# Performance work log

Hardware: AMD Instinct MI355X
Metric: run time of the kernel (lower is better)

Reference implementation:

```python
import jax, jax.numpy as jnp
import numpy as np

T, B, N, C, H, D = 4, 8, 1024, 512, 8, 64
EPS = 1e-5


def setup_inputs() -> dict:
    key = jax.random.key(0)
    ks = jax.random.split(key, 16)
    d = {"x": jax.random.normal(ks[0], (T, B, N, C), jnp.float32)}
    for i, nm in enumerate(["q", "k", "v", "p"]):
        kW, kmu, kvar = jax.random.split(ks[1 + i], 3)
        d[f"W{nm}"] = jax.random.normal(kW, (C, C), jnp.float32) * 0.02
        d[f"b{nm}"] = jnp.zeros((C,), jnp.float32)
        d[f"g{nm}"] = jnp.ones((C,), jnp.float32)
        d[f"beta{nm}"] = jnp.zeros((C,), jnp.float32)
        d[f"mu{nm}"] = jax.random.normal(kmu, (C,), jnp.float32) * 0.1
        d[f"var{nm}"] = jax.random.uniform(kvar, (C,), jnp.float32, 0.5, 1.5)
    return d


def _lin_bn(z, W, b, g, beta, mu, var):
    # nn.Linear over channel dim, then eval-mode BatchNorm1d per channel
    y = jnp.einsum('tbnc,dc->tbnd', z, W) + b
    return (y - mu) * (g * jax.lax.rsqrt(var + EPS)) + beta


def _to_heads(z):
    # (t,b,n,c) -> (t,b,h,n,d)
    return z.reshape(T, B, N, H, D).transpose(0, 1, 3, 2, 4)


def reference(x, Wq, bq, gq, betaq, muq, varq,
              Wk, bk, gk, betak, muk, vark,
              Wv, bv, gv, betav, muv, varv,
              Wp, bp, gp, betap, mup, varp):
    q = _to_heads(_lin_bn(x, Wq, bq, gq, betaq, muq, varq))
    k = _to_heads(_lin_bn(x, Wk, bk, gk, betak, muk, vark))
    v = _to_heads(_lin_bn(x, Wv, bv, gv, betav, muv, varv))
    # attention_linear variant: kv = (k^T @ v) / N ; y = q @ kv
    kv = jnp.einsum('tbhnd,tbhne->tbhde', k, v) / float(N)  # (t,b,h,d,d)
    y = jnp.einsum('tbhnd,tbhde->tbhne', q, kv)             # (t,b,h,n,d)
    y = y.transpose(0, 1, 3, 2, 4).reshape(T, B, N, C)
    return _lin_bn(y, Wp, bp, gp, betap, mup, varp)
```

## Files before the change

### kernel.cpp

```cpp
#include <hip/hip_runtime.h>

#define T_ 4
#define B_ 8
#define N_ 1024
#define C_ 512
#define H_ 8
#define D_ 64
#define M_ (T_*B_*N_)
#define TB_ (T_*B_)

typedef __bf16 bf16;
typedef __bf16 bf16x4 __attribute__((ext_vector_type(4)));
typedef __bf16 bf16x8 __attribute__((ext_vector_type(8)));
typedef float f32x4 __attribute__((ext_vector_type(4)));

__device__ __forceinline__ void gload16(const void* g, void* l) {
  __builtin_amdgcn_global_load_lds(
      (const __attribute__((address_space(1))) void*)g,
      (__attribute__((address_space(3))) void*)l, 16, 0, 0);
}

struct PtrPack { const float* p[24]; };

__global__ __launch_bounds__(256)
void prep_all(PtrPack pk, bf16* __restrict__ WB, float* __restrict__ BS) {
  const int mat = blockIdx.x >> 9, d = blockIdx.x & 511;
  const float* W    = pk.p[6*mat + 0];
  const float* b    = pk.p[6*mat + 1];
  const float* g    = pk.p[6*mat + 2];
  const float* beta = pk.p[6*mat + 3];
  const float* mu   = pk.p[6*mat + 4];
  const float* var  = pk.p[6*mat + 5];
  float s = g[d] * rsqrtf(var[d] + 1e-5f);
  if (threadIdx.x == 0) BS[mat*512 + d] = (b[d] - mu[d]) * s + beta[d];
  bf16* Wout = WB + (size_t)mat * 262144 + (size_t)d * 512;
  for (int c = threadIdx.x; c < 512; c += 256)
    Wout[c] = (bf16)(W[(size_t)d * 512 + c] * s);
}

__global__ __launch_bounds__(256)
void prep_wqT(const float* __restrict__ W, const float* __restrict__ g,
              const float* __restrict__ var, bf16* __restrict__ WqT) {
  const int di = blockIdx.x >> 3, ci = blockIdx.x & 7;
  const int t = threadIdx.x;
  __shared__ float lds[64][65];
  const int rgrp = t >> 4, k = t & 15;
#pragma unroll
  for (int p = 0; p < 4; p++) {
    int r = p * 16 + rgrp;
    int d = di * 64 + r;
    float s = g[d] * rsqrtf(var[d] + 1e-5f);
    float4 v = *(const float4*)(W + (size_t)d * 512 + ci * 64 + k * 4);
    lds[r][k*4+0] = v.x * s; lds[r][k*4+1] = v.y * s;
    lds[r][k*4+2] = v.z * s; lds[r][k*4+3] = v.w * s;
  }
  __syncthreads();
#pragma unroll
  for (int p = 0; p < 16; p++) {
    int c = p * 4 + (t >> 6), dd = t & 63;
    WqT[(size_t)(ci*64 + c) * 512 + di*64 + dd] = (bf16)lds[dd][c];
  }
}

__global__ __launch_bounds__(256)
void cvt_x_t(const float* __restrict__ x, bf16* __restrict__ xb,
             bf16* __restrict__ xT, float* __restrict__ spart) {
  const int bid = blockIdx.x;
  const int tb = bid >> 7, nc = (bid >> 3) & 15, cc = bid & 7;
  const int t = threadIdx.x;
  __shared__ float lds[64][65];
  __shared__ float sred[16][64];
  const float* xbase = x + (size_t)tb * 524288 + (size_t)nc * 64 * 512 + cc * 64;
  bf16* xbb = xb + (size_t)tb * 524288 + (size_t)nc * 64 * 512 + cc * 64;
  bf16* xTb = xT + (size_t)tb * 524288 + (size_t)(cc * 64) * 1024 + nc * 64;
  const int rgrp = t >> 4, k = t & 15;
  float s0 = 0, s1 = 0, s2 = 0, s3 = 0;
#pragma unroll
  for (int p = 0; p < 4; p++) {
    int r = p * 16 + rgrp;
    float4 v = *(const float4*)(xbase + (size_t)r * 512 + k * 4);
    bf16x4 o; o[0]=(bf16)v.x; o[1]=(bf16)v.y; o[2]=(bf16)v.z; o[3]=(bf16)v.w;
    *(bf16x4*)(xbb + (size_t)r * 512 + k * 4) = o;
    lds[r][k*4+0]=v.x; lds[r][k*4+1]=v.y; lds[r][k*4+2]=v.z; lds[r][k*4+3]=v.w;
    s0 += v.x; s1 += v.y; s2 += v.z; s3 += v.w;
  }
  sred[rgrp][k*4+0]=s0; sred[rgrp][k*4+1]=s1; sred[rgrp][k*4+2]=s2; sred[rgrp][k*4+3]=s3;
  __syncthreads();
#pragma unroll
  for (int p = 0; p < 16; p++) {
    int c = p * 4 + (t >> 6), n = t & 63;
    xTb[(size_t)c * 1024 + n] = (bf16)lds[n][c];
  }
  if (t < 64) {
    float tot = 0;
#pragma unroll
    for (int rg = 0; rg < 16; rg++) tot += sred[rg][t];
    spart[(size_t)((tb*8 + cc)*16 + nc) * 64 + t] = tot;
  }
}

__global__ __launch_bounds__(512)
void ksvs(const bf16* __restrict__ WB, const float* __restrict__ spart,
          float* __restrict__ ksv) {
  const int tb = blockIdx.x, m = blockIdx.y;
  const int c = threadIdx.x, cc = c >> 6, cl = c & 63;
  __shared__ float sl[512];
  float tot = 0;
#pragma unroll
  for (int ncf = 0; ncf < 16; ncf++)
    tot += spart[(size_t)((tb*8 + cc)*16 + ncf) * 64 + cl];
  sl[c] = tot;
  __syncthreads();
  const bf16* Wrow = WB + (size_t)(m + 1) * 262144 + (size_t)c * 512;
  float acc = 0;
  for (int k = 0; k < 512; k += 8) {
    bf16x8 wv = *(const bf16x8*)(Wrow + k);
#pragma unroll
    for (int i = 0; i < 8; i++) acc += (float)wv[i] * sl[k + i];
  }
  ksv[m * 16384 + tb * 512 + c] = acc;
}

template <int NKT, int MT, int NT, bool BF16OUT, bool BIAS2, bool SYM>
__global__ __launch_bounds__(256)
void gemm2(const bf16* __restrict__ Abase, size_t Astr,
           const bf16* __restrict__ Btbase, size_t Btstr,
           const float* __restrict__ BSb, const float* __restrict__ cpart,
           bf16* __restrict__ ob, float* __restrict__ of, size_t Ostr) {
  constexpr int K = NKT * 64;
  constexpr int PERB = SYM ? (MT * (MT + 1) / 2) : (MT * NT);
  const int bid = blockIdx.x;
  const int xcd = bid & 7, j9 = bid >> 3;
  const int bat = xcd + 8 * (j9 / PERB);
  const int tile = j9 % PERB;
  int mi, ni;
  if constexpr (SYM) {
    if (tile < 4)      { mi = 0; ni = tile; }
    else if (tile < 7) { mi = 1; ni = tile - 3; }
    else if (tile < 9) { mi = 2; ni = tile - 5; }
    else               { mi = 3; ni = 3; }
  } else { mi = tile / NT; ni = tile % NT; }
  const bf16* A = Abase + (size_t)bat * Astr;
  const bf16* Bt = Btbase + (size_t)bat * Btstr;
  const int m0 = mi * 128, n0 = ni * 128;
  __shared__ __align__(16) bf16 As[2][128][64];
  __shared__ __align__(16) bf16 Bs[2][128][64];
  const int tid = threadIdx.x, w = tid >> 6, l = tid & 63;
  const int wm = w >> 1, wn = w & 1;
  const int lr = l & 15, lq = l >> 4, l7 = l & 7, lh = l >> 3;
  const int srcc = (l7 ^ lh) * 8;
  f32x4 acc[4][4] = {};

#define STG2(buf, kt)                                                         \
  { _Pragma("unroll") for (int i_ = 0; i_ < 4; i_++) {                        \
      int rb_ = w * 32 + i_ * 8;                                              \
      gload16(A  + (size_t)(m0 + rb_ + lh) * K + (kt) * 64 + srcc,            \
              &As[buf][rb_][0]);                                              \
      gload16(Bt + (size_t)(n0 + rb_ + lh) * K + (kt) * 64 + srcc,            \
              &Bs[buf][rb_][0]); } }

  STG2(0, 0);
  __syncthreads();
  for (int kt = 0; kt < NKT; kt++) {
    const int cur = kt & 1;
    if (kt + 1 < NKT) STG2(cur ^ 1, kt + 1);
    bf16x8 af[4][2], bv[4][2];
#pragma unroll
    for (int f = 0; f < 4; f++) {
      int ra = wm * 64 + f * 16 + lr, rb2 = wn * 64 + f * 16 + lr;
#pragma unroll
      for (int s = 0; s < 2; s++) {
        af[f][s] = *(const bf16x8*)&As[cur][ra][((s*4+lq) ^ (ra & 7)) * 8];
        bv[f][s] = *(const bf16x8*)&Bs[cur][rb2][((s*4+lq) ^ (rb2 & 7)) * 8];
      }
    }
#pragma unroll
    for (int mt = 0; mt < 4; mt++)
#pragma unroll
      for (int nt = 0; nt < 4; nt++)
#pragma unroll
        for (int s = 0; s < 2; s++)
          acc[mt][nt] = __builtin_amdgcn_mfma_f32_16x16x32_bf16(
              af[mt][s], bv[nt][s], acc[mt][nt], 0, 0, 0);
    __syncthreads();
  }
#undef STG2

  const int ldo = NT * 128;
#pragma unroll
  for (int mt = 0; mt < 4; mt++)
#pragma unroll
    for (int nt = 0; nt < 4; nt++) {
      int j = n0 + wn * 64 + nt * 16 + lr;
      float bj = 0.f;
      if constexpr (BIAS2) {
        bj = BSb[1536 + j];
#pragma unroll
        for (int h = 0; h < 8; h++)
          bj += cpart[(size_t)(bat * 8 + h) * 512 + j];
      }
      size_t mrow = (size_t)m0 + wm * 64 + mt * 16 + lq * 4;
#pragma unroll
      for (int r = 0; r < 4; r++) {
        if constexpr (BF16OUT)
          ob[(size_t)bat * Ostr + (mrow + r) * ldo + j] = (bf16)(acc[mt][nt][r] + bj);
        else
          of[(size_t)bat * Ostr + (mrow + r) * ldo + j] = acc[mt][nt][r] + bj;
      }
    }

  if constexpr (SYM) {
    if (mi != ni) {
      bf16* TB = (bf16*)As;
      __syncthreads();
#pragma unroll
      for (int mt = 0; mt < 4; mt++)
#pragma unroll
        for (int nt = 0; nt < 4; nt++) {
          int a = wn * 64 + nt * 16 + lr;
#pragma unroll
          for (int r = 0; r < 4; r++) {
            int b = wm * 64 + mt * 16 + lq * 4 + r;
            TB[(a * 128 + b) ^ ((a & 7) << 3)] = (bf16)acc[mt][nt][r];
          }
        }
      __syncthreads();
      const int a = tid >> 1, half = tid & 1;
#pragma unroll
      for (int i = 0; i < 4; i++) {
        int a2 = a + (i >> 1) * 64;
        int c8 = half * 8 + (i & 1) * 4;
        (void)a2; (void)c8;
      }
#pragma unroll
      for (int i = 0; i < 8; i++) {
        int rowa = tid >> 1;
        int c8 = half * 8 + i;
        bf16x8 v = *(const bf16x8*)&TB[(rowa * 128 + c8 * 8) ^ ((rowa & 7) << 3)];
        *(bf16x8*)(ob + (size_t)bat * Ostr + (size_t)(ni * 128 + rowa) * ldo +
                   mi * 128 + c8 * 8) = v;
      }
    }
  }
}

__global__ __launch_bounds__(256)
void kvz(const bf16* __restrict__ KGb, const bf16* __restrict__ WB,
         const float* __restrict__ BS, const float* __restrict__ ksv,
         bf16* __restrict__ ZT, float* __restrict__ cpart) {
  const int gid = blockIdx.x, tb = gid >> 3, h = gid & 7;
  const int t = threadIdx.x, w = t >> 6, l = t & 63;
  const int lr = l & 15, lq = l >> 4;
  __shared__ __align__(16) char lds[65536 + 65536 + 8192];
  bf16* bufA = (bf16*)lds;
  bf16* bufV = (bf16*)(lds + 65536);
  bf16* kvb  = (bf16*)(lds + 131072);

#pragma unroll
  for (int i = 0; i < 16; i++) {
    int r = i * 4 + w;
    gload16(KGb + (size_t)tb * 262144 + (size_t)(64*h + r) * 512 + ((l ^ (r & 7)) * 8),
            bufA + r * 512);
    gload16(WB + 2u * 262144 + (size_t)(64*h + r) * 512 + ((l ^ (r & 7)) * 8),
            bufV + r * 512);
  }
  __syncthreads();

  f32x4 acc2[4][4] = {};
#pragma unroll
  for (int ks = 0; ks < 4; ks++) {
    int gch = w * 16 + ks * 4 + lq;
    bf16x8 af2[4], bv2[4];
#pragma unroll
    for (int mf = 0; mf < 4; mf++) {
      int d = mf * 16 + lr;
      af2[mf] = *(const bf16x8*)&bufA[d * 512 + ((gch ^ (d & 7)) * 8)];
    }
#pragma unroll
    for (int nf = 0; nf < 4; nf++) {
      int e = nf * 16 + lr;
      bv2[nf] = *(const bf16x8*)&bufV[e * 512 + ((gch ^ (e & 7)) * 8)];
    }
#pragma unroll
    for (int mf = 0; mf < 4; mf++)
#pragma unroll
      for (int nf = 0; nf < 4; nf++)
        acc2[mf][nf] = __builtin_amdgcn_mfma_f32_16x16x32_bf16(
            af2[mf], bv2[nf], acc2[mf][nf], 0, 0, 0);
  }
  __syncthreads();

  float* part = (float*)lds + w * 4096;
#pragma unroll
  for (int mf = 0; mf < 4; mf++)
#pragma unroll
    for (int nf = 0; nf < 4; nf++)
#pragma unroll
      for (int r = 0; r < 4; r++) {
        int d = mf * 16 + lq * 4 + r, e = nf * 16 + lr;
        part[d * 64 + e] = acc2[mf][nf][r];
      }
  __syncthreads();
  {
    const float inv = 1.f / 1024.f;
    const float* pb = (const float*)lds;
#pragma unroll
    for (int jj = 0; jj < 16; jj++) {
      int flat = jj * 256 + t, d = flat >> 6, e = flat & 63;
      float s = pb[flat] + pb[4096 + flat] + pb[8192 + flat] + pb[12288 + flat];
      float ksh = ksv[tb * 512 + 64*h + d];
      float vsh = ksv[16384 + tb * 512 + 64*h + e];
      float bkh = BS[512 + 64*h + d];
      float bvh = BS[1024 + 64*h + e];
      float kv = (s + ksh * bvh + bkh * vsh) * inv + bkh * bvh;
      kvb[d * 64 + (((e >> 3) ^ (d & 7)) * 8 + (e & 7))] = (bf16)kv;
    }
  }
  __syncthreads();

#pragma unroll
  for (int i = 0; i < 16; i++) {
    int rb = i * 32 + w * 8;
    int r = rb + (l >> 3);
    gload16(WB + 3u * 262144 + (size_t)r * 512 + 64*h + (((l & 7) ^ (r & 7)) * 8),
            bufA + rb * 64);
  }
  __syncthreads();

  f32x4 acc3[4][8] = {};
#pragma unroll
  for (int s = 0; s < 2; s++) {
    bf16x8 af3[4];
#pragma unroll
    for (int mf = 0; mf < 4; mf++) {
      int d = mf * 16 + lr;
      af3[mf] = *(const bf16x8*)&kvb[d * 64 + (((s*4+lq) ^ (d & 7)) * 8)];
    }
#pragma unroll
    for (int nf = 0; nf < 8; nf++) {
      int jj = w * 128 + nf * 16 + lr;
      bf16x8 b3 = *(const bf16x8*)&bufA[jj * 64 + (((s*4+lq) ^ (jj & 7)) * 8)];
#pragma unroll
      for (int mf = 0; mf < 4; mf++)
        acc3[mf][nf] = __builtin_amdgcn_mfma_f32_16x16x32_bf16(
            af3[mf], b3, acc3[mf][nf], 0, 0, 0);
    }
  }

  bf16* zbase = ZT + (size_t)tb * 262144 + 64*h;
#pragma unroll
  for (int nf = 0; nf < 8; nf++) {
    int jj = w * 128 + nf * 16 + lr;
    float cp = 0.f;
#pragma unroll
    for (int mf = 0; mf < 4; mf++) {
      bf16x4 o;
#pragma unroll
      for (int r = 0; r < 4; r++) {
        o[r] = (bf16)acc3[mf][nf][r];
        cp += acc3[mf][nf][r] * BS[64*h + mf*16 + lq*4 + r];
      }
      *(bf16x4*)(zbase + (size_t)jj * 512 + mf * 16 + lq * 4) = o;
    }
    cp += __shfl_xor(cp, 16);
    cp += __shfl_xor(cp, 32);
    if (lq == 0) cpart[(size_t)(tb * 8 + h) * 512 + jj] = cp;
  }
}

extern "C" void kernel_launch(void* const* d_in, const int* in_sizes, int n_in,
                              void* d_out, int out_size, void* d_ws, size_t ws_size,
                              hipStream_t stream) {
  const float* x = (const float*)d_in[0];
  char* ws = (char*)d_ws;
  bf16*  xb    = (bf16*)(ws + 0);
  bf16*  xT    = (bf16*)(ws + 33554432);
  bf16*  Gb    = (bf16*)(ws + 67108864);
  bf16*  KGb   = (bf16*)(ws + 83886080);
  bf16*  ZT    = (bf16*)(ws + 100663296);
  bf16*  VT    = (bf16*)(ws + 117440512);
  bf16*  WB    = (bf16*)(ws + 134217728);
  bf16*  WqT   = (bf16*)(ws + 136314880);
  float* BS    = (float*)(ws + 136839168);
  float* ksv   = (float*)(ws + 136847360);
  float* cpart = (float*)(ws + 136978432);
  float* spart = (float*)(ws + 137502720);
  (void)in_sizes; (void)n_in; (void)out_size; (void)ws_size;

  PtrPack pk;
  for (int i = 0; i < 24; i++) pk.p[i] = (const float*)d_in[1 + i];

  prep_all<<<2048, 256, 0, stream>>>(pk, WB, BS);
  prep_wqT<<<64, 256, 0, stream>>>((const float*)d_in[1], (const float*)d_in[3],
                                   (const float*)d_in[6], WqT);
  cvt_x_t<<<4096, 256, 0, stream>>>(x, xb, xT, spart);
  ksvs<<<dim3(32, 2), 512, 0, stream>>>(WB, spart, ksv);
  gemm2<16, 4, 4, true, false, true><<<320, 256, 0, stream>>>(
      xT, 524288, xT, 524288, nullptr, nullptr, Gb, nullptr, 262144);
  gemm2<8, 4, 4, true, false, false><<<512, 256, 0, stream>>>(
      WB + 262144, 0, Gb, 262144, nullptr, nullptr, KGb, nullptr, 262144);
  kvz<<<256, 256, 0, stream>>>(KGb, WB, BS, ksv, ZT, cpart);
  gemm2<8, 4, 4, true, false, false><<<512, 256, 0, stream>>>(
      ZT, 262144, WqT, 0, nullptr, nullptr, VT, nullptr, 262144);
  gemm2<8, 8, 4, false, true, false><<<1024, 256, 0, stream>>>(
      xb, 524288, VT, 262144, BS, cpart, nullptr, (float*)d_out, 524288);
}
```

Before: 149.7 us.

## Drop LDS double buffering in GEMMs and use 512-thread 256x128 final GEMM

The batched GEMM kernel switches from double-buffered LDS staging to a single buffer with load, sync, compute, sync per k-step. This halves LDS use per block so more blocks can be resident. The final output GEMM moves to a new 512-thread kernel with 256x128 tiles, which reuses each B tile across twice as many rows and hoists the bias sums out of the store loop. The cost is that load latency is no longer overlapped with MFMA work inside a block, so hiding it now relies on occupancy.

```diff
diff --git a/kernel.cpp b/kernel.cpp
--- a/kernel.cpp
+++ b/kernel.cpp
@@ -121,12 +121,11 @@
   ksv[m * 16384 + tb * 512 + c] = acc;
 }
 
-template <int NKT, int MT, int NT, bool BF16OUT, bool BIAS2, bool SYM>
+template <int NKT, int MT, int NT, bool BF16OUT, bool SYM>
 __global__ __launch_bounds__(256)
-void gemm2(const bf16* __restrict__ Abase, size_t Astr,
-           const bf16* __restrict__ Btbase, size_t Btstr,
-           const float* __restrict__ BSb, const float* __restrict__ cpart,
-           bf16* __restrict__ ob, float* __restrict__ of, size_t Ostr) {
+void gemm_b(const bf16* __restrict__ Abase, size_t Astr,
+            const bf16* __restrict__ Btbase, size_t Btstr,
+            bf16* __restrict__ ob, float* __restrict__ of, size_t Ostr) {
   constexpr int K = NKT * 64;
   constexpr int PERB = SYM ? (MT * (MT + 1) / 2) : (MT * NT);
   const int bid = blockIdx.x;
@@ -143,35 +142,29 @@
   const bf16* A = Abase + (size_t)bat * Astr;
   const bf16* Bt = Btbase + (size_t)bat * Btstr;
   const int m0 = mi * 128, n0 = ni * 128;
-  __shared__ __align__(16) bf16 As[2][128][64];
-  __shared__ __align__(16) bf16 Bs[2][128][64];
+  __shared__ __align__(16) bf16 As[128][64];
+  __shared__ __align__(16) bf16 Bs[128][64];
   const int tid = threadIdx.x, w = tid >> 6, l = tid & 63;
   const int wm = w >> 1, wn = w & 1;
   const int lr = l & 15, lq = l >> 4, l7 = l & 7, lh = l >> 3;
   const int srcc = (l7 ^ lh) * 8;
   f32x4 acc[4][4] = {};
-
-#define STG2(buf, kt)                                                         \
-  { _Pragma("unroll") for (int i_ = 0; i_ < 4; i_++) {                        \
-      int rb_ = w * 32 + i_ * 8;                                              \
-      gload16(A  + (size_t)(m0 + rb_ + lh) * K + (kt) * 64 + srcc,            \
-              &As[buf][rb_][0]);                                              \
-      gload16(Bt + (size_t)(n0 + rb_ + lh) * K + (kt) * 64 + srcc,            \
-              &Bs[buf][rb_][0]); } }
-
-  STG2(0, 0);
-  __syncthreads();
   for (int kt = 0; kt < NKT; kt++) {
-    const int cur = kt & 1;
-    if (kt + 1 < NKT) STG2(cur ^ 1, kt + 1);
+#pragma unroll
+    for (int i = 0; i < 4; i++) {
+      int rb = w * 32 + i * 8;
+      gload16(A  + (size_t)(m0 + rb + lh) * K + kt * 64 + srcc, &As[rb][0]);
+      gload16(Bt + (size_t)(n0 + rb + lh) * K + kt * 64 + srcc, &Bs[rb][0]);
+    }
+    __syncthreads();
     bf16x8 af[4][2], bv[4][2];
 #pragma unroll
     for (int f = 0; f < 4; f++) {
       int ra = wm * 64 + f * 16 + lr, rb2 = wn * 64 + f * 16 + lr;
 #pragma unroll
       for (int s = 0; s < 2; s++) {
-        af[f][s] = *(const bf16x8*)&As[cur][ra][((s*4+lq) ^ (ra & 7)) * 8];
-        bv[f][s] = *(const bf16x8*)&Bs[cur][rb2][((s*4+lq) ^ (rb2 & 7)) * 8];
+        af[f][s] = *(const bf16x8*)&As[ra][((s*4+lq) ^ (ra & 7)) * 8];
+        bv[f][s] = *(const bf16x8*)&Bs[rb2][((s*4+lq) ^ (rb2 & 7)) * 8];
       }
     }
 #pragma unroll
@@ -184,28 +177,19 @@
               af[mt][s], bv[nt][s], acc[mt][nt], 0, 0, 0);
     __syncthreads();
   }
-#undef STG2
-
   const int ldo = NT * 128;
 #pragma unroll
   for (int mt = 0; mt < 4; mt++)
 #pragma unroll
     for (int nt = 0; nt < 4; nt++) {
       int j = n0 + wn * 64 + nt * 16 + lr;
-      float bj = 0.f;
-      if constexpr (BIAS2) {
-        bj = BSb[1536 + j];
-#pragma unroll
-        for (int h = 0; h < 8; h++)
-          bj += cpart[(size_t)(bat * 8 + h) * 512 + j];
-      }
       size_t mrow = (size_t)m0 + wm * 64 + mt * 16 + lq * 4;
 #pragma unroll
       for (int r = 0; r < 4; r++) {
         if constexpr (BF16OUT)
-          ob[(size_t)bat * Ostr + (mrow + r) * ldo + j] = (bf16)(acc[mt][nt][r] + bj);
+          ob[(size_t)bat * Ostr + (mrow + r) * ldo + j] = (bf16)acc[mt][nt][r];
         else
-          of[(size_t)bat * Ostr + (mrow + r) * ldo + j] = acc[mt][nt][r] + bj;
+          of[(size_t)bat * Ostr + (mrow + r) * ldo + j] = acc[mt][nt][r];
       }
     }
 
@@ -225,16 +209,9 @@
           }
         }
       __syncthreads();
-      const int a = tid >> 1, half = tid & 1;
-#pragma unroll
-      for (int i = 0; i < 4; i++) {
-        int a2 = a + (i >> 1) * 64;
-        int c8 = half * 8 + (i & 1) * 4;
-        (void)a2; (void)c8;
-      }
+      const int rowa = tid >> 1, half = tid & 1;
 #pragma unroll
       for (int i = 0; i < 8; i++) {
-        int rowa = tid >> 1;
         int c8 = half * 8 + i;
         bf16x8 v = *(const bf16x8*)&TB[(rowa * 128 + c8 * 8) ^ ((rowa & 7) << 3)];
         *(bf16x8*)(ob + (size_t)bat * Ostr + (size_t)(ni * 128 + rowa) * ldo +
@@ -242,6 +219,82 @@
       }
     }
   }
+}
+
+__global__ __launch_bounds__(512)
+void gemm_w(const bf16* __restrict__ Abase, size_t Astr,
+            const bf16* __restrict__ Btbase, size_t Btstr,
+            const float* __restrict__ BSb, const float* __restrict__ cpart,
+            float* __restrict__ of, size_t Ostr) {
+  constexpr int K = 512, NKT = 8;
+  constexpr int PERB = 16;
+  const int bid = blockIdx.x;
+  const int xcd = bid & 7, j9 = bid >> 3;
+  const int bat = xcd + 8 * (j9 / PERB);
+  const int tile = j9 % PERB;
+  const int mi = tile >> 2, ni = tile & 3;
+  const bf16* A = Abase + (size_t)bat * Astr;
+  const bf16* Bt = Btbase + (size_t)bat * Btstr;
+  const int m0 = mi * 256, n0 = ni * 128;
+  __shared__ __align__(16) bf16 As[256][64];
+  __shared__ __align__(16) bf16 Bs[128][64];
+  const int tid = threadIdx.x, w = tid >> 6, l = tid & 63;
+  const int wm = w >> 1, wn = w & 1;
+  const int lr = l & 15, lq = l >> 4, l7 = l & 7, lh = l >> 3;
+  const int srcc = (l7 ^ lh) * 8;
+  f32x4 acc[4][4] = {};
+  for (int kt = 0; kt < NKT; kt++) {
+#pragma unroll
+    for (int i = 0; i < 4; i++) {
+      int rb = w * 32 + i * 8;
+      gload16(A + (size_t)(m0 + rb + lh) * K + kt * 64 + srcc, &As[rb][0]);
+    }
+#pragma unroll
+    for (int i = 0; i < 2; i++) {
+      int rb = w * 16 + i * 8;
+      gload16(Bt + (size_t)(n0 + rb + lh) * K + kt * 64 + srcc, &Bs[rb][0]);
+    }
+    __syncthreads();
+    bf16x8 af[4][2], bv[4][2];
+#pragma unroll
+    for (int f = 0; f < 4; f++) {
+      int ra = wm * 64 + f * 16 + lr, rb2 = wn * 64 + f * 16 + lr;
+#pragma unroll
+      for (int s = 0; s < 2; s++) {
+        af[f][s] = *(const bf16x8*)&As[ra][((s*4+lq) ^ (ra & 7)) * 8];
+        bv[f][s] = *(const bf16x8*)&Bs[rb2][((s*4+lq) ^ (rb2 & 7)) * 8];
+      }
+    }
+#pragma unroll
+    for (int mt = 0; mt < 4; mt++)
+#pragma unroll
+      for (int nt = 0; nt < 4; nt++)
+#pragma unroll
+        for (int s = 0; s < 2; s++)
+          acc[mt][nt] = __builtin_amdgcn_mfma_f32_16x16x32_bf16(
+              af[mt][s], bv[nt][s], acc[mt][nt], 0, 0, 0);
+    __syncthreads();
+  }
+  float bja[4];
+#pragma unroll
+  for (int nt = 0; nt < 4; nt++) {
+    int j = n0 + wn * 64 + nt * 16 + lr;
+    float bj = BSb[1536 + j];
+#pragma unroll
+    for (int h = 0; h < 8; h++)
+      bj += cpart[(size_t)(bat * 8 + h) * 512 + j];
+    bja[nt] = bj;
+  }
+#pragma unroll
+  for (int mt = 0; mt < 4; mt++)
+#pragma unroll
+    for (int nt = 0; nt < 4; nt++) {
+      int j = n0 + wn * 64 + nt * 16 + lr;
+      size_t mrow = (size_t)m0 + wm * 64 + mt * 16 + lq * 4;
+#pragma unroll
+      for (int r = 0; r < 4; r++)
+        of[(size_t)bat * Ostr + (mrow + r) * 512 + j] = acc[mt][nt][r] + bja[nt];
+    }
 }
 
 __global__ __launch_bounds__(256)
@@ -395,13 +448,13 @@
                                    (const float*)d_in[6], WqT);
   cvt_x_t<<<4096, 256, 0, stream>>>(x, xb, xT, spart);
   ksvs<<<dim3(32, 2), 512, 0, stream>>>(WB, spart, ksv);
-  gemm2<16, 4, 4, true, false, true><<<320, 256, 0, stream>>>(
-      xT, 524288, xT, 524288, nullptr, nullptr, Gb, nullptr, 262144);
-  gemm2<8, 4, 4, true, false, false><<<512, 256, 0, stream>>>(
-      WB + 262144, 0, Gb, 262144, nullptr, nullptr, KGb, nullptr, 262144);
+  gemm_b<16, 4, 4, true, true><<<320, 256, 0, stream>>>(
+      xT, 524288, xT, 524288, Gb, nullptr, 262144);
+  gemm_b<8, 4, 4, true, false><<<512, 256, 0, stream>>>(
+      WB + 262144, 0, Gb, 262144, KGb, nullptr, 262144);
   kvz<<<256, 256, 0, stream>>>(KGb, WB, BS, ksv, ZT, cpart);
-  gemm2<8, 4, 4, true, false, false><<<512, 256, 0, stream>>>(
-      ZT, 262144, WqT, 0, nullptr, nullptr, VT, nullptr, 262144);
-  gemm2<8, 8, 4, false, true, false><<<1024, 256, 0, stream>>>(
-      xb, 524288, VT, 262144, BS, cpart, nullptr, (float*)d_out, 524288);
-}
+  gemm_b<8, 4, 4, true, false><<<512, 256, 0, stream>>>(
+      ZT, 262144, WqT, 0, VT, nullptr, 262144);
+  gemm_w<<<512, 512, 0, stream>>>(
+      xb, 524288, VT, 262144, BS, cpart, (float*)d_out, 524288);
+}
```

Measured after the change: 150.5 us. Within noise of the previous version (+0.5%).

## Replace double-buffered symmetric GEMM with smaller single-buffered 64x128 tiles

Applied to the files above, without the earlier changes.

The GEMM kernel changes from 128x128 tiles with double-buffered LDS staging to 64x128 tiles with a single LDS buffer, doubling the block count of every launch. It also drops the symmetric Gram-matrix path that computed only upper-triangle tiles and wrote transposes, so the x^T x GEMM now computes every tile. The aim is more blocks and lower LDS use for higher occupancy. The cost is lost load/compute overlap, less reuse per tile, and redundant work on the symmetric product.

```diff
diff --git a/kernel.cpp b/kernel.cpp
--- a/kernel.cpp
+++ b/kernel.cpp
@@ -121,61 +121,58 @@
   ksv[m * 16384 + tb * 512 + c] = acc;
 }
 
-template <int NKT, int MT, int NT, bool BF16OUT, bool BIAS2, bool SYM>
-__global__ __launch_bounds__(256)
-void gemm2(const bf16* __restrict__ Abase, size_t Astr,
-           const bf16* __restrict__ Btbase, size_t Btstr,
-           const float* __restrict__ BSb, const float* __restrict__ cpart,
-           bf16* __restrict__ ob, float* __restrict__ of, size_t Ostr) {
+template <int NKT, int MTILES, bool BF16OUT, bool BIAS>
+__global__ __launch_bounds__(256)
+void gemm_n(const bf16* __restrict__ Abase, size_t Astr,
+            const bf16* __restrict__ Btbase, size_t Btstr,
+            const float* __restrict__ BSb, const float* __restrict__ cpart,
+            bf16* __restrict__ ob, float* __restrict__ of, size_t Ostr) {
   constexpr int K = NKT * 64;
-  constexpr int PERB = SYM ? (MT * (MT + 1) / 2) : (MT * NT);
+  constexpr int PERB = MTILES * 4;
   const int bid = blockIdx.x;
   const int xcd = bid & 7, j9 = bid >> 3;
   const int bat = xcd + 8 * (j9 / PERB);
   const int tile = j9 % PERB;
-  int mi, ni;
-  if constexpr (SYM) {
-    if (tile < 4)      { mi = 0; ni = tile; }
-    else if (tile < 7) { mi = 1; ni = tile - 3; }
-    else if (tile < 9) { mi = 2; ni = tile - 5; }
-    else               { mi = 3; ni = 3; }
-  } else { mi = tile / NT; ni = tile % NT; }
+  const int mi = tile >> 2, ni = tile & 3;
   const bf16* A = Abase + (size_t)bat * Astr;
   const bf16* Bt = Btbase + (size_t)bat * Btstr;
-  const int m0 = mi * 128, n0 = ni * 128;
-  __shared__ __align__(16) bf16 As[2][128][64];
-  __shared__ __align__(16) bf16 Bs[2][128][64];
+  const int m0 = mi * 64, n0 = ni * 128;
+  __shared__ __align__(16) bf16 As[64][64];
+  __shared__ __align__(16) bf16 Bs[128][64];
   const int tid = threadIdx.x, w = tid >> 6, l = tid & 63;
   const int wm = w >> 1, wn = w & 1;
   const int lr = l & 15, lq = l >> 4, l7 = l & 7, lh = l >> 3;
   const int srcc = (l7 ^ lh) * 8;
-  f32x4 acc[4][4] = {};
-
-#define STG2(buf, kt)                                                         \
-  { _Pragma("unroll") for (int i_ = 0; i_ < 4; i_++) {                        \
-      int rb_ = w * 32 + i_ * 8;                                              \
-      gload16(A  + (size_t)(m0 + rb_ + lh) * K + (kt) * 64 + srcc,            \
-              &As[buf][rb_][0]);                                              \
-      gload16(Bt + (size_t)(n0 + rb_ + lh) * K + (kt) * 64 + srcc,            \
-              &Bs[buf][rb_][0]); } }
-
-  STG2(0, 0);
-  __syncthreads();
+  f32x4 acc[2][4] = {};
   for (int kt = 0; kt < NKT; kt++) {
-    const int cur = kt & 1;
-    if (kt + 1 < NKT) STG2(cur ^ 1, kt + 1);
-    bf16x8 af[4][2], bv[4][2];
+#pragma unroll
+    for (int i = 0; i < 2; i++) {
+      int rb = w * 16 + i * 8;
+      gload16(A + (size_t)(m0 + rb + lh) * K + kt * 64 + srcc, &As[rb][0]);
+    }
+#pragma unroll
+    for (int i = 0; i < 4; i++) {
+      int rb = w * 32 + i * 8;
+      gload16(Bt + (size_t)(n0 + rb + lh) * K + kt * 64 + srcc, &Bs[rb][0]);
+    }
+    __syncthreads();
+    bf16x8 af[2][2], bv[4][2];
+#pragma unroll
+    for (int f = 0; f < 2; f++) {
+      int ra = wm * 32 + f * 16 + lr;
+#pragma unroll
+      for (int s = 0; s < 2; s++)
+        af[f][s] = *(const bf16x8*)&As[ra][((s*4+lq) ^ (ra & 7)) * 8];
+    }
 #pragma unroll
     for (int f = 0; f < 4; f++) {
-      int ra = wm * 64 + f * 16 + lr, rb2 = wn * 64 + f * 16 + lr;
-#pragma unroll
-      for (int s = 0; s < 2; s++) {
-        af[f][s] = *(const bf16x8*)&As[cur][ra][((s*4+lq) ^ (ra & 7)) * 8];
-        bv[f][s] = *(const bf16x8*)&Bs[cur][rb2][((s*4+lq) ^ (rb2 & 7)) * 8];
-      }
-    }
-#pragma unroll
-    for (int mt = 0; mt < 4; mt++)
+      int rb2 = wn * 64 + f * 16 + lr;
+#pragma unroll
+      for (int s = 0; s < 2; s++)
+        bv[f][s] = *(const bf16x8*)&Bs[rb2][((s*4+lq) ^ (rb2 & 7)) * 8];
+    }
+#pragma unroll
+    for (int mt = 0; mt < 2; mt++)
 #pragma unroll
       for (int nt = 0; nt < 4; nt++)
 #pragma unroll
@@ -184,64 +181,34 @@
               af[mt][s], bv[nt][s], acc[mt][nt], 0, 0, 0);
     __syncthreads();
   }
-#undef STG2
-
-  const int ldo = NT * 128;
-#pragma unroll
-  for (int mt = 0; mt < 4; mt++)
+
+  float bja[4];
+  if constexpr (BIAS) {
 #pragma unroll
     for (int nt = 0; nt < 4; nt++) {
       int j = n0 + wn * 64 + nt * 16 + lr;
-      float bj = 0.f;
-      if constexpr (BIAS2) {
-        bj = BSb[1536 + j];
-#pragma unroll
-        for (int h = 0; h < 8; h++)
-          bj += cpart[(size_t)(bat * 8 + h) * 512 + j];
-      }
-      size_t mrow = (size_t)m0 + wm * 64 + mt * 16 + lq * 4;
+      float bj = BSb[1536 + j];
+#pragma unroll
+      for (int h = 0; h < 8; h++)
+        bj += cpart[(size_t)(bat * 8 + h) * 512 + j];
+      bja[nt] = bj;
+    }
+  }
+#pragma unroll
+  for (int mt = 0; mt < 2; mt++)
+#pragma unroll
+    for (int nt = 0; nt < 4; nt++) {
+      int j = n0 + wn * 64 + nt * 16 + lr;
+      size_t mrow = (size_t)m0 + wm * 32 + mt * 16 + lq * 4;
 #pragma unroll
       for (int r = 0; r < 4; r++) {
         if constexpr (BF16OUT)
-          ob[(size_t)bat * Ostr + (mrow + r) * ldo + j] = (bf16)(acc[mt][nt][r] + bj);
+          ob[(size_t)bat * Ostr + (mrow + r) * 512 + j] = (bf16)acc[mt][nt][r];
         else
-          of[(size_t)bat * Ostr + (mrow + r) * ldo + j] = acc[mt][nt][r] + bj;
+          of[(size_t)bat * Ostr + (mrow + r) * 512 + j] =
+              acc[mt][nt][r] + (BIAS ? bja[nt] : 0.f);
       }
     }
-
-  if constexpr (SYM) {
-    if (mi != ni) {
-      bf16* TB = (bf16*)As;
-      __syncthreads();
-#pragma unroll
-      for (int mt = 0; mt < 4; mt++)
-#pragma unroll
-        for (int nt = 0; nt < 4; nt++) {
-          int a = wn * 64 + nt * 16 + lr;
-#pragma unroll
-          for (int r = 0; r < 4; r++) {
-            int b = wm * 64 + mt * 16 + lq * 4 + r;
-            TB[(a * 128 + b) ^ ((a & 7) << 3)] = (bf16)acc[mt][nt][r];
-          }
-        }
-      __syncthreads();
-      const int a = tid >> 1, half = tid & 1;
-#pragma unroll
-      for (int i = 0; i < 4; i++) {
-        int a2 = a + (i >> 1) * 64;
-        int c8 = half * 8 + (i & 1) * 4;
-        (void)a2; (void)c8;
-      }
-#pragma unroll
-      for (int i = 0; i < 8; i++) {
-        int rowa = tid >> 1;
-        int c8 = half * 8 + i;
-        bf16x8 v = *(const bf16x8*)&TB[(rowa * 128 + c8 * 8) ^ ((rowa & 7) << 3)];
-        *(bf16x8*)(ob + (size_t)bat * Ostr + (size_t)(ni * 128 + rowa) * ldo +
-                   mi * 128 + c8 * 8) = v;
-      }
-    }
-  }
 }
 
 __global__ __launch_bounds__(256)
@@ -395,13 +362,13 @@
                                    (const float*)d_in[6], WqT);
   cvt_x_t<<<4096, 256, 0, stream>>>(x, xb, xT, spart);
   ksvs<<<dim3(32, 2), 512, 0, stream>>>(WB, spart, ksv);
-  gemm2<16, 4, 4, true, false, true><<<320, 256, 0, stream>>>(
+  gemm_n<16, 8, true, false><<<1024, 256, 0, stream>>>(
       xT, 524288, xT, 524288, nullptr, nullptr, Gb, nullptr, 262144);
-  gemm2<8, 4, 4, true, false, false><<<512, 256, 0, stream>>>(
+  gemm_n<8, 8, true, false><<<1024, 256, 0, stream>>>(
       WB + 262144, 0, Gb, 262144, nullptr, nullptr, KGb, nullptr, 262144);
   kvz<<<256, 256, 0, stream>>>(KGb, WB, BS, ksv, ZT, cpart);
-  gemm2<8, 4, 4, true, false, false><<<512, 256, 0, stream>>>(
+  gemm_n<8, 8, true, false><<<1024, 256, 0, stream>>>(
       ZT, 262144, WqT, 0, nullptr, nullptr, VT, nullptr, 262144);
-  gemm2<8, 8, 4, false, true, false><<<1024, 256, 0, stream>>>(
+  gemm_n<8, 16, false, true><<<2048, 256, 0, stream>>>(
       xb, 524288, VT, 262144, BS, cpart, nullptr, (float*)d_out, 524288);
 }
```

Result: faster. 144.2 us (-3.7%).
